# Kernel tuning notes

Hardware: AMD Instinct MI355X
Metric: run time of the kernel (lower is better)

Reference implementation:

```python
import jax, jax.numpy as jnp
import numpy as np

EMB = 2048
HEADS = 16
HEAD_DIM = EMB // HEADS
MIN_WINDOW = 64
MAX_WINDOW = 256
ROPE_BASE = 10000.0


def setup_inputs() -> dict:
    key = jax.random.key(0)
    ks = jax.random.split(key, 5)
    B, S = 2, 2048
    x = jax.random.normal(ks[0], (B, S, EMB), dtype=jnp.float32)
    w_qkv = jax.random.normal(ks[1], (3 * EMB, EMB), dtype=jnp.float32) * (EMB ** -0.5)
    w_out = jax.random.normal(ks[2], (EMB, EMB), dtype=jnp.float32) * (EMB ** -0.5)
    w_c1 = jax.random.normal(ks[3], (EMB // 4, EMB), dtype=jnp.float32) * 0.1 * (EMB ** -0.5)
    w_c2 = jax.random.normal(ks[4], (1, EMB // 4), dtype=jnp.float32) * 0.1 * ((EMB // 4) ** -0.5)
    return {"x": x, "w_qkv": w_qkv, "w_out": w_out, "w_c1": w_c1, "w_c2": w_c2}


def _rotate_half(t):
    # interleaved pairs: [-x1, x0, -x3, x2, ...]
    x1 = t[..., ::2]
    x2 = t[..., 1::2]
    return jnp.stack((-x2, x1), axis=-1).reshape(t.shape)


def _rope_tables(seq_len, dtype):
    inv_freq = 1.0 / (ROPE_BASE ** (jnp.arange(0, HEAD_DIM, 2, dtype=jnp.float32) / HEAD_DIM))
    pos = jnp.arange(seq_len, dtype=jnp.float32)
    freqs = jnp.outer(pos, inv_freq)                      # [S, D/2]
    emb = jnp.concatenate([freqs, freqs], axis=-1)        # [S, D]
    return jnp.cos(emb)[None, None].astype(dtype), jnp.sin(emb)[None, None].astype(dtype)


def _forward(x, w_qkv, w_out, w_c1, w_c2):
    B, S, _ = x.shape
    scale = HEAD_DIM ** -0.5

    qkv = x @ w_qkv.T                                     # [B, S, 3E]
    qkv = qkv.reshape(B, S, 3, HEADS, HEAD_DIM).transpose(2, 0, 3, 1, 4)
    q, k, v = qkv[0], qkv[1], qkv[2]                      # each [B, H, S, D]

    cos, sin = _rope_tables(S, x.dtype)
    q = q * cos + _rotate_half(q) * sin
    k = k * cos + _rotate_half(k) * sin

    scores = jnp.einsum("bhqd,bhkd->bhqk", q, k) * scale  # [B, H, S, S]

    # adaptive window size from input complexity
    var = jnp.var(x.reshape(B, -1), axis=1, ddof=1)        # torch unbiased var over dims [1,2]
    var_norm = jax.nn.sigmoid(var * 10.0 - 5.0)
    x_mean = x.mean(axis=1)                                # [B, E]
    hidden = jax.nn.silu(x_mean @ w_c1.T)
    learned = jax.nn.sigmoid(hidden @ w_c2.T)[:, 0]        # [B]
    complexity = (var_norm + learned) / 2.0
    window_f = MIN_WINDOW + complexity * (MAX_WINDOW - MIN_WINDOW)
    window = window_f.mean().astype(jnp.int32)             # trunc like .int()
    window = jnp.maximum(jnp.minimum(window, S), MIN_WINDOW)

    # causal + sliding-window mask: keep 0 <= q_pos - k_pos < window
    pos = jnp.arange(S)
    rel = pos[:, None] - pos[None, :]                      # [S, S]
    keep = (rel >= 0) & (rel < window)
    scores = jnp.where(keep[None, None], scores, -jnp.inf)

    attn = jax.nn.softmax(scores, axis=-1)
    out = jnp.einsum("bhqk,bhkd->bhqd", attn, v)           # [B, H, S, D]
    out = out.transpose(0, 2, 1, 3).reshape(B, S, EMB)
    return out @ w_out.T


def reference(x, w_qkv, w_out, w_c1, w_c2):
    return _forward(x, w_qkv, w_out, w_c1, w_c2)
```

## Files before the change

kernel.cpp:

```cpp
#include <hip/hip_runtime.h>
#include <math.h>


#define S_LEN 2048
#define EMB 2048
#define HEADS 16
#define HDIM 128
#define NT 20
#define PSTR 336

typedef _Float16 f16x8 __attribute__((ext_vector_type(8)));
typedef _Float16 f16x4 __attribute__((ext_vector_type(4)));
typedef _Float16 f16x2 __attribute__((ext_vector_type(2)));
typedef float f32x4 __attribute__((ext_vector_type(4)));

__device__ __forceinline__ void gld16(const void* g, void* l) {
    __builtin_amdgcn_global_load_lds(
        (const __attribute__((address_space(1))) unsigned int*)g,
        (__attribute__((address_space(3))) unsigned int*)l, 16, 0, 0);
}

__global__ void rope_table(float* __restrict__ ctab, float* __restrict__ stab) {
    int s = blockIdx.x;
    int d = threadIdx.x;
    int j = d & 63;
    double inv = pow(10000.0, -(double)j / 64.0);
    double ang = (double)s * inv;
    ctab[s * HDIM + d] = (float)cos(ang);
    stab[s * HDIM + d] = (float)sin(ang);
}

__global__ __launch_bounds__(256) void col_reduce(const float* __restrict__ x,
                                                  float* __restrict__ xmean_acc,
                                                  double* __restrict__ scal) {
    int b = blockIdx.z;
    int cg = blockIdx.x;
    int sg = blockIdx.y;
    int e = cg * 256 + threadIdx.x;
    const float* xb = x + ((size_t)b * S_LEN + sg * 256) * EMB;
    double csum = 0.0, csq = 0.0;
    for (int s = 0; s < 256; ++s) {
        float v = xb[(size_t)s * EMB + e];
        csum += v;
        csq += (double)v * (double)v;
    }
    atomicAdd(xmean_acc + b * EMB + e, (float)csum);
    __shared__ double rs[256], rq[256];
    rs[threadIdx.x] = csum; rq[threadIdx.x] = csq;
    __syncthreads();
    for (int off = 128; off > 0; off >>= 1) {
        if (threadIdx.x < off) {
            rs[threadIdx.x] += rs[threadIdx.x + off];
            rq[threadIdx.x] += rq[threadIdx.x + off];
        }
        __syncthreads();
    }
    if (threadIdx.x == 0) {
        atomicAdd(&scal[b], rs[0]);
        atomicAdd(&scal[2 + b], rq[0]);
    }
}

__global__ __launch_bounds__(256) void hidden_kernel(const float* __restrict__ xmean_acc,
                                                     const float* __restrict__ wc1,
                                                     float* __restrict__ hidden) {
    int j = blockIdx.x;
    int b = blockIdx.y;
    const float* xm = xmean_acc + b * EMB;
    const float* wr = wc1 + (size_t)j * EMB;
    double acc = 0.0;
    for (int k = threadIdx.x; k < EMB; k += 256)
        acc += (double)xm[k] * (double)wr[k];
    __shared__ double red[256];
    red[threadIdx.x] = acc;
    __syncthreads();
    for (int off = 128; off > 0; off >>= 1) {
        if (threadIdx.x < off) red[threadIdx.x] += red[threadIdx.x + off];
        __syncthreads();
    }
    if (threadIdx.x == 0) {
        double z = red[0] * (1.0 / 2048.0);
        hidden[b * 512 + j] = (float)(z / (1.0 + exp(-z)));
    }
}

__global__ __launch_bounds__(512) void window_kernel(const float* __restrict__ hidden,
                                                     const float* __restrict__ wc2,
                                                     const double* __restrict__ scal,
                                                     int* __restrict__ wout) {
    __shared__ double red[512];
    __shared__ double wfs[2];
    for (int b = 0; b < 2; ++b) {
        red[threadIdx.x] = (double)hidden[b * 512 + threadIdx.x] * (double)wc2[threadIdx.x];
        __syncthreads();
        for (int off = 256; off > 0; off >>= 1) {
            if (threadIdx.x < off) red[threadIdx.x] += red[threadIdx.x + off];
            __syncthreads();
        }
        if (threadIdx.x == 0) {
            double pre = red[0];
            double learned = 1.0 / (1.0 + exp(-pre));
            const double N = (double)S_LEN * (double)EMB;
            double sum = scal[b], sq = scal[2 + b];
            double var = (sq - sum * sum / N) / (N - 1.0);
            double vn = 1.0 / (1.0 + exp(-(var * 10.0 - 5.0)));
            double comp = 0.5 * (vn + learned);
            wfs[b] = 64.0 + comp * 192.0;
        }
        __syncthreads();
    }
    if (threadIdx.x == 0) {
        float wf = (float)(0.5 * (wfs[0] + wfs[1]));
        int w = (int)wf;
        if (w > S_LEN) w = S_LEN;
        if (w < 64) w = 64;
        *wout = w;
    }
}

__global__ __launch_bounds__(256) void cvt_f16(const float* __restrict__ s,
                                               _Float16* __restrict__ d, int n4) {
    int i = blockIdx.x * 256 + threadIdx.x;
    if (i < n4) {
        float4 v = ((const float4*)s)[i];
        f16x4 o;
        o.x = (_Float16)v.x; o.y = (_Float16)v.y;
        o.z = (_Float16)v.z; o.w = (_Float16)v.w;
        ((f16x4*)d)[i] = o;
    }
}

#define GEMM_PROLOGUE(An, Wn)                                                   \
    __shared__ _Float16 As[128 * 32];                                           \
    __shared__ _Float16 Bs[128 * 32];                                           \
    const int tid = threadIdx.x;                                                \
    const int lane = tid & 63;                                                  \
    const int wv = tid >> 6;                                                    \
    const int wm = wv >> 1, wn = wv & 1;                                        \
    const int m0 = blockIdx.y * 128;                                            \
    const int n0 = blockIdx.x * 128;                                            \
    const int srow = wv * 32 + (lane >> 2);                                     \
    const int scol = (lane & 3) * 8;                                            \
    const _Float16* agp = An + (size_t)(m0 + srow) * EMB + scol;                \
    const _Float16* bgp = Wn + (size_t)(n0 + srow) * EMB + scol;                \
    _Float16* al = &As[(wv * 32) * 32];                                         \
    _Float16* bl = &Bs[(wv * 32) * 32];                                         \
    const int frow = lane & 15;                                                 \
    const int fcol = (lane >> 4) * 8;                                           \
    f32x4 acc[4][4] = {};                                                       \
    for (int k0 = 0; k0 < EMB; k0 += 32) {                                      \
        __syncthreads();                                                        \
        gld16(agp, al);                                                         \
        gld16(agp + 16 * EMB, al + 16 * 32);                                    \
        gld16(bgp, bl);                                                         \
        gld16(bgp + 16 * EMB, bl + 16 * 32);                                    \
        agp += 32; bgp += 32;                                                   \
        __syncthreads();                                                        \
        f16x8 af[4], bf[4];                                                     \
        _Pragma("unroll")                                                       \
        for (int i = 0; i < 4; ++i)                                             \
            af[i] = *(const f16x8*)&As[(wm * 64 + i * 16 + frow) * 32 + fcol];  \
        _Pragma("unroll")                                                       \
        for (int j = 0; j < 4; ++j)                                             \
            bf[j] = *(const f16x8*)&Bs[(wn * 64 + j * 16 + frow) * 32 + fcol];  \
        _Pragma("unroll")                                                       \
        for (int i = 0; i < 4; ++i)                                             \
            _Pragma("unroll")                                                   \
            for (int j = 0; j < 4; ++j)                                         \
                acc[i][j] = __builtin_amdgcn_mfma_f32_16x16x32_f16(             \
                    af[i], bf[j], acc[i][j], 0, 0, 0);                          \
    }                                                                           \
    const int colbase = lane & 15;                                              \
    const int rowoff = (lane >> 4) * 4;

__global__ __launch_bounds__(256) void gemm_qkv_f16(const _Float16* __restrict__ An,
                                                    const _Float16* __restrict__ Wn,
                                                    float* __restrict__ qb,
                                                    float* __restrict__ kb,
                                                    _Float16* __restrict__ vt) {
    GEMM_PROLOGUE(An, Wn)
    const int which = n0 >> 11;
    const int h = (n0 >> 7) & 15;
    if (which == 2) {
#pragma unroll
        for (int i = 0; i < 4; ++i) {
#pragma unroll
            for (int j = 0; j < 4; ++j) {
                const int d = wn * 64 + j * 16 + colbase;
                int m = m0 + wm * 64 + i * 16 + rowoff;
                int b = m >> 11, s = m & 2047;
                f16x4 o;
#pragma unroll
                for (int r = 0; r < 4; ++r) o[r] = (_Float16)acc[i][j][r];
                *(f16x4*)&vt[(((size_t)b * HEADS + h) * HDIM + d) * S_LEN + s] = o;
            }
        }
    } else {
        float* dst = which == 0 ? qb : kb;
#pragma unroll
        for (int i = 0; i < 4; ++i) {
#pragma unroll
            for (int j = 0; j < 4; ++j) {
                const int d = wn * 64 + j * 16 + colbase;
#pragma unroll
                for (int r = 0; r < 4; ++r) {
                    int m = m0 + wm * 64 + i * 16 + rowoff + r;
                    int b = m >> 11, s = m & 2047;
                    dst[(((size_t)b * HEADS + h) * S_LEN + s) * HDIM + d] = acc[i][j][r];
                }
            }
        }
    }
}

__global__ __launch_bounds__(256) void gemm_out_f16(const _Float16* __restrict__ An,
                                                    const _Float16* __restrict__ Wn,
                                                    float* __restrict__ C) {
    GEMM_PROLOGUE(An, Wn)
#pragma unroll
    for (int i = 0; i < 4; ++i) {
#pragma unroll
        for (int j = 0; j < 4; ++j) {
            const int n = n0 + wn * 64 + j * 16 + colbase;
#pragma unroll
            for (int r = 0; r < 4; ++r) {
                int m = m0 + wm * 64 + i * 16 + rowoff + r;
                C[(size_t)m * EMB + n] = acc[i][j][r];
            }
        }
    }
}

__global__ __launch_bounds__(256) void rope_apply(const float* __restrict__ qb,
                                                  const float* __restrict__ kb,
                                                  _Float16* __restrict__ q16,
                                                  _Float16* __restrict__ k16,
                                                  const float* __restrict__ ctab,
                                                  const float* __restrict__ stab) {
    size_t idx = (size_t)blockIdx.x * 256 + threadIdx.x;
    int i = idx & 63;
    int s = (int)((idx >> 6) & 2047);
    size_t bh = idx >> 17;
    int d0 = i * 2;
    size_t base = (bh * S_LEN + s) * HDIM + d0;
    float c0 = ctab[s * HDIM + d0], c1 = ctab[s * HDIM + d0 + 1];
    float s0 = stab[s * HDIM + d0], s1 = stab[s * HDIM + d0 + 1];
    float2 q = *(const float2*)(qb + base);
    float2 k = *(const float2*)(kb + base);
    f16x2 qo, ko;
    qo.x = (_Float16)(q.x * c0 - q.y * s0);
    qo.y = (_Float16)(q.y * c1 + q.x * s1);
    ko.x = (_Float16)(k.x * c0 - k.y * s0);
    ko.y = (_Float16)(k.y * c1 + k.x * s1);
    *(f16x2*)(q16 + base) = qo;
    *(f16x2*)(k16 + base) = ko;
}

__global__ __launch_bounds__(256) void attn_mfma(const _Float16* __restrict__ q16,
                                                 const _Float16* __restrict__ k16,
                                                 const _Float16* __restrict__ v16t,
                                                 _Float16* __restrict__ ob,
                                                 const int* __restrict__ wptr) {
    const int q0 = blockIdx.x * 64;
    const int h = blockIdx.y;
    const int b = blockIdx.z;
    const int tid = threadIdx.x;
    const int lane = tid & 63;
    const int wv = tid >> 6;
    const int w = *wptr;

    __shared__ _Float16 Pl[4][16 * PSTR];
    _Float16* Pw = Pl[wv];

    const int kstart = q0 - 256;
    int ntlo_w = (257 - w) >> 4;
    int ntlo_n = q0 < 256 ? ((256 - q0) >> 4) : 0;
    const int ntlo = ntlo_w > ntlo_n ? ntlo_w : ntlo_n;

    const int frow = lane & 15;
    const int fgrp = lane >> 4;
    const int fcol = fgrp * 8;

    const size_t bh = (size_t)b * HEADS + h;
    const _Float16* Qp = q16 + (bh * S_LEN + q0 + wv * 16 + frow) * HDIM + fcol;
    const _Float16* Kb = k16 + bh * S_LEN * HDIM;
    const _Float16* Vt = v16t + bh * HDIM * S_LEN;

    f16x8 aq[4];
#pragma unroll
    for (int ks = 0; ks < 4; ++ks) aq[ks] = *(const f16x8*)(Qp + ks * 32);

    f32x4 accs[NT];
#pragma unroll
    for (int nt = 0; nt < NT; ++nt) accs[nt] = (f32x4){0.f, 0.f, 0.f, 0.f};
#pragma unroll
    for (int nt = 0; nt < NT; ++nt) {
        if (nt < ntlo) continue;
        int krow = kstart + nt * 16 + frow;
        if (krow < 0) krow = 0;
        const _Float16* kp = Kb + (size_t)krow * HDIM + fcol;
#pragma unroll
        for (int ks = 0; ks < 4; ++ks) {
            f16x8 bk = *(const f16x8*)(kp + ks * 32);
            accs[nt] = __builtin_amdgcn_mfma_f32_16x16x32_f16(aq[ks], bk, accs[nt], 0, 0, 0);
        }
    }

    const int qrow = fgrp * 4;
    const int qabs = q0 + wv * 16 + qrow;
    const float scale = 0.08838834764831845f;
    float mx[4] = {-INFINITY, -INFINITY, -INFINITY, -INFINITY};
#pragma unroll
    for (int nt = 0; nt < NT; ++nt) {
        int key = kstart + nt * 16 + frow;
#pragma unroll
        for (int r = 0; r < 4; ++r) {
            int rel = (qabs + r) - key;
            bool keep = (key >= 0) && (rel >= 0) && (rel < w);
            float s = keep ? accs[nt][r] * scale : -INFINITY;
            accs[nt][r] = s;
            mx[r] = fmaxf(mx[r], s);
        }
    }
#pragma unroll
    for (int r = 0; r < 4; ++r) {
        float m = mx[r];
#pragma unroll
        for (int off = 1; off < 16; off <<= 1)
            m = fmaxf(m, __shfl_xor(m, off, 64));
        mx[r] = m;
    }

    float ls[4] = {0.f, 0.f, 0.f, 0.f};
#pragma unroll
    for (int nt = 0; nt < NT; ++nt) {
#pragma unroll
        for (int r = 0; r < 4; ++r) {
            float p = __expf(accs[nt][r] - mx[r]);
            ls[r] += p;
            Pw[(qrow + r) * PSTR + nt * 16 + frow] = (_Float16)p;
        }
    }
    float inv[4];
#pragma unroll
    for (int r = 0; r < 4; ++r) {
        float l = ls[r];
#pragma unroll
        for (int off = 1; off < 16; off <<= 1)
            l += __shfl_xor(l, off, 64);
        inv[r] = 1.f / l;
    }

    const int pvlo = ntlo >> 1;
    f32x4 acco[8];
#pragma unroll
    for (int jt = 0; jt < 8; ++jt) acco[jt] = (f32x4){0.f, 0.f, 0.f, 0.f};
    const _Float16* Pr = &Pl[wv][frow * PSTR];
#pragma unroll
    for (int kp = 0; kp < 10; ++kp) {
        if (kp < pvlo) continue;
        f16x8 ap = *(const f16x8*)(Pr + kp * 32 + fcol);
        int kv = kstart + kp * 32 + fcol;
        if (kv < 0) kv = 0;
#pragma unroll
        for (int jt = 0; jt < 8; ++jt) {
            f16x8 bv = *(const f16x8*)(Vt + (size_t)(jt * 16 + frow) * S_LEN + kv);
            acco[jt] = __builtin_amdgcn_mfma_f32_16x16x32_f16(ap, bv, acco[jt], 0, 0, 0);
        }
    }

#pragma unroll
    for (int jt = 0; jt < 8; ++jt) {
#pragma unroll
        for (int r = 0; r < 4; ++r) {
            int s = qabs + r;
            ob[((size_t)b * S_LEN + s) * EMB + h * HDIM + jt * 16 + frow] =
                (_Float16)(acco[jt][r] * inv[r]);
        }
    }
}

extern "C" void kernel_launch(void* const* d_in, const int* in_sizes, int n_in,
                              void* d_out, int out_size, void* d_ws, size_t ws_size,
                              hipStream_t stream) {
    const float* x     = (const float*)d_in[0];
    const float* w_qkv = (const float*)d_in[1];
    const float* w_out = (const float*)d_in[2];
    const float* w_c1  = (const float*)d_in[3];
    const float* w_c2  = (const float*)d_in[4];
    float* out = (float*)d_out;
    char* ws = (char*)d_ws;

    double*    scal   = (double*)(ws + 0);
    int*       win    = (int*)(ws + 64);
    float*     xmean  = (float*)(ws + 128);
    float*     hidden = (float*)(ws + 16640);
    float*     ctab   = (float*)(ws + 32768);
    float*     stab   = (float*)(ws + 32768 + 1048576);
    float*     qb     = (float*)(ws + 4194304);
    float*     kb     = (float*)(ws + 37748736);
    _Float16*  wqkv16 = (_Float16*)(ws + 71303168);
    _Float16*  x16    = (_Float16*)(ws + 96468992);
    _Float16*  v16t   = (_Float16*)(ws + 113246208);
    _Float16*  q16    = (_Float16*)(ws + 71303168);
    _Float16*  k16    = (_Float16*)(ws + 96468992);
    _Float16*  ao16   = (_Float16*)(ws + 4194304);
    _Float16*  wout16 = (_Float16*)(ws + 37748736);

    hipMemsetAsync(d_ws, 0, 32768, stream);

    rope_table<<<dim3(S_LEN), dim3(HDIM), 0, stream>>>(ctab, stab);
    col_reduce<<<dim3(8, 8, 2), dim3(256), 0, stream>>>(x, xmean, scal);
    hidden_kernel<<<dim3(512, 2), dim3(256), 0, stream>>>(xmean, w_c1, hidden);
    window_kernel<<<dim3(1), dim3(512), 0, stream>>>(hidden, w_c2, scal, win);

    cvt_f16<<<dim3(8192), dim3(256), 0, stream>>>(x, x16, 2097152);
    cvt_f16<<<dim3(12288), dim3(256), 0, stream>>>(w_qkv, wqkv16, 3145728);

    gemm_qkv_f16<<<dim3(48, 32), dim3(256), 0, stream>>>(x16, wqkv16, qb, kb, v16t);
    rope_apply<<<dim3(16384), dim3(256), 0, stream>>>(qb, kb, q16, k16, ctab, stab);
    attn_mfma<<<dim3(32, HEADS, 2), dim3(256), 0, stream>>>(q16, k16, v16t, ao16, win);

    cvt_f16<<<dim3(4096), dim3(256), 0, stream>>>(w_out, wout16, 1048576);
    gemm_out_f16<<<dim3(16, 32), dim3(256), 0, stream>>>(ao16, wout16, out);
}
```

Baseline: 477.6 us.

## Fuse RoPE into QKV GEMM epilogue and x fp16 conversion into column reduce

Applies RoPE directly in the QKV GEMM epilogue, using a lane-xor shuffle to fetch each element's pair partner and an interleaved cos/sin table, then writes fp16 q/k. This removes the fp32 q/k intermediates and the separate rope_apply pass. The x-to-fp16 conversion is folded into col_reduce, which already reads x, so one cvt launch goes away. The workspace layout is reorganised around the smaller buffers. The epilogue now does more per-element work (shuffle, table load, scalar fp16 stores), which may cost some GEMM time.

```diff
diff --git a/kernel.cpp b/kernel.cpp
--- a/kernel.cpp
+++ b/kernel.cpp
@@ -11,7 +11,6 @@
 
 typedef _Float16 f16x8 __attribute__((ext_vector_type(8)));
 typedef _Float16 f16x4 __attribute__((ext_vector_type(4)));
-typedef _Float16 f16x2 __attribute__((ext_vector_type(2)));
 typedef float f32x4 __attribute__((ext_vector_type(4)));
 
 __device__ __forceinline__ void gld16(const void* g, void* l) {
@@ -20,27 +19,30 @@
         (__attribute__((address_space(3))) unsigned int*)l, 16, 0, 0);
 }
 
-__global__ void rope_table(float* __restrict__ ctab, float* __restrict__ stab) {
+__global__ void rope_table(float2* __restrict__ cstab) {
     int s = blockIdx.x;
     int d = threadIdx.x;
     int j = d & 63;
     double inv = pow(10000.0, -(double)j / 64.0);
     double ang = (double)s * inv;
-    ctab[s * HDIM + d] = (float)cos(ang);
-    stab[s * HDIM + d] = (float)sin(ang);
+    cstab[s * HDIM + d] = make_float2((float)cos(ang), (float)sin(ang));
 }
 
 __global__ __launch_bounds__(256) void col_reduce(const float* __restrict__ x,
                                                   float* __restrict__ xmean_acc,
-                                                  double* __restrict__ scal) {
+                                                  double* __restrict__ scal,
+                                                  _Float16* __restrict__ x16) {
     int b = blockIdx.z;
     int cg = blockIdx.x;
     int sg = blockIdx.y;
     int e = cg * 256 + threadIdx.x;
-    const float* xb = x + ((size_t)b * S_LEN + sg * 256) * EMB;
+    const size_t base = ((size_t)b * S_LEN + sg * 256) * EMB;
+    const float* xb = x + base;
+    _Float16* xo = x16 + base;
     double csum = 0.0, csq = 0.0;
     for (int s = 0; s < 256; ++s) {
         float v = xb[(size_t)s * EMB + e];
+        xo[(size_t)s * EMB + e] = (_Float16)v;
         csum += v;
         csq += (double)v * (double)v;
     }
@@ -175,9 +177,10 @@
 
 __global__ __launch_bounds__(256) void gemm_qkv_f16(const _Float16* __restrict__ An,
                                                     const _Float16* __restrict__ Wn,
-                                                    float* __restrict__ qb,
-                                                    float* __restrict__ kb,
-                                                    _Float16* __restrict__ vt) {
+                                                    _Float16* __restrict__ q16,
+                                                    _Float16* __restrict__ k16,
+                                                    _Float16* __restrict__ vt,
+                                                    const float2* __restrict__ cstab) {
     GEMM_PROLOGUE(An, Wn)
     const int which = n0 >> 11;
     const int h = (n0 >> 7) & 15;
@@ -196,7 +199,8 @@
             }
         }
     } else {
-        float* dst = which == 0 ? qb : kb;
+        _Float16* dst = which == 0 ? q16 : k16;
+        const float sgn = (colbase & 1) ? 1.f : -1.f;
 #pragma unroll
         for (int i = 0; i < 4; ++i) {
 #pragma unroll
@@ -206,7 +210,11 @@
                 for (int r = 0; r < 4; ++r) {
                     int m = m0 + wm * 64 + i * 16 + rowoff + r;
                     int b = m >> 11, s = m & 2047;
-                    dst[(((size_t)b * HEADS + h) * S_LEN + s) * HDIM + d] = acc[i][j][r];
+                    float a = acc[i][j][r];
+                    float p = __shfl_xor(a, 1, 64);
+                    float2 cs = cstab[(size_t)s * HDIM + d];
+                    float o = fmaf(a, cs.x, sgn * p * cs.y);
+                    dst[(((size_t)b * HEADS + h) * S_LEN + s) * HDIM + d] = (_Float16)o;
                 }
             }
         }
@@ -229,31 +237,6 @@
             }
         }
     }
-}
-
-__global__ __launch_bounds__(256) void rope_apply(const float* __restrict__ qb,
-                                                  const float* __restrict__ kb,
-                                                  _Float16* __restrict__ q16,
-                                                  _Float16* __restrict__ k16,
-                                                  const float* __restrict__ ctab,
-                                                  const float* __restrict__ stab) {
-    size_t idx = (size_t)blockIdx.x * 256 + threadIdx.x;
-    int i = idx & 63;
-    int s = (int)((idx >> 6) & 2047);
-    size_t bh = idx >> 17;
-    int d0 = i * 2;
-    size_t base = (bh * S_LEN + s) * HDIM + d0;
-    float c0 = ctab[s * HDIM + d0], c1 = ctab[s * HDIM + d0 + 1];
-    float s0 = stab[s * HDIM + d0], s1 = stab[s * HDIM + d0 + 1];
-    float2 q = *(const float2*)(qb + base);
-    float2 k = *(const float2*)(kb + base);
-    f16x2 qo, ko;
-    qo.x = (_Float16)(q.x * c0 - q.y * s0);
-    qo.y = (_Float16)(q.y * c1 + q.x * s1);
-    ko.x = (_Float16)(k.x * c0 - k.y * s0);
-    ko.y = (_Float16)(k.y * c1 + k.x * s1);
-    *(f16x2*)(q16 + base) = qo;
-    *(f16x2*)(k16 + base) = ko;
 }
 
 __global__ __launch_bounds__(256) void attn_mfma(const _Float16* __restrict__ q16,
@@ -395,32 +378,26 @@
     int*       win    = (int*)(ws + 64);
     float*     xmean  = (float*)(ws + 128);
     float*     hidden = (float*)(ws + 16640);
-    float*     ctab   = (float*)(ws + 32768);
-    float*     stab   = (float*)(ws + 32768 + 1048576);
-    float*     qb     = (float*)(ws + 4194304);
-    float*     kb     = (float*)(ws + 37748736);
-    _Float16*  wqkv16 = (_Float16*)(ws + 71303168);
-    _Float16*  x16    = (_Float16*)(ws + 96468992);
-    _Float16*  v16t   = (_Float16*)(ws + 113246208);
-    _Float16*  q16    = (_Float16*)(ws + 71303168);
-    _Float16*  k16    = (_Float16*)(ws + 96468992);
-    _Float16*  ao16   = (_Float16*)(ws + 4194304);
-    _Float16*  wout16 = (_Float16*)(ws + 37748736);
+    float2*    cstab  = (float2*)(ws + 32768);
+    _Float16*  x16    = (_Float16*)(ws + 4194304);
+    _Float16*  wqkv16 = (_Float16*)(ws + 20971520);
+    _Float16*  ao16   = (_Float16*)(ws + 20971520);
+    _Float16*  v16t   = (_Float16*)(ws + 46137344);
+    _Float16*  q16    = (_Float16*)(ws + 62914560);
+    _Float16*  k16    = (_Float16*)(ws + 79691776);
+    _Float16*  wout16 = (_Float16*)(ws + 96468992);
 
     hipMemsetAsync(d_ws, 0, 32768, stream);
 
-    rope_table<<<dim3(S_LEN), dim3(HDIM), 0, stream>>>(ctab, stab);
-    col_reduce<<<dim3(8, 8, 2), dim3(256), 0, stream>>>(x, xmean, scal);
+    rope_table<<<dim3(S_LEN), dim3(HDIM), 0, stream>>>(cstab);
+    col_reduce<<<dim3(8, 8, 2), dim3(256), 0, stream>>>(x, xmean, scal, x16);
     hidden_kernel<<<dim3(512, 2), dim3(256), 0, stream>>>(xmean, w_c1, hidden);
     window_kernel<<<dim3(1), dim3(512), 0, stream>>>(hidden, w_c2, scal, win);
 
-    cvt_f16<<<dim3(8192), dim3(256), 0, stream>>>(x, x16, 2097152);
     cvt_f16<<<dim3(12288), dim3(256), 0, stream>>>(w_qkv, wqkv16, 3145728);
-
-    gemm_qkv_f16<<<dim3(48, 32), dim3(256), 0, stream>>>(x16, wqkv16, qb, kb, v16t);
-    rope_apply<<<dim3(16384), dim3(256), 0, stream>>>(qb, kb, q16, k16, ctab, stab);
+    cvt_f16<<<dim3(4096), dim3(256), 0, stream>>>(w_out, wout16, 1048576);
+
+    gemm_qkv_f16<<<dim3(48, 32), dim3(256), 0, stream>>>(x16, wqkv16, q16, k16, v16t, cstab);
     attn_mfma<<<dim3(32, HEADS, 2), dim3(256), 0, stream>>>(q16, k16, v16t, ao16, win);
-
-    cvt_f16<<<dim3(4096), dim3(256), 0, stream>>>(w_out, wout16, 1048576);
     gemm_out_f16<<<dim3(16, 32), dim3(256), 0, stream>>>(ao16, wout16, out);
 }
```

New measurement: 462.3 us. -3.2%, faster.
